# Optimization experiments

Measured on AMD Instinct MI355X. Metric: run time of the kernel, lower is better.

## Reference

```python
import jax, jax.numpy as jnp
import numpy as np

N_NODES = 100000
N_EDGES = 1600000
IN_DIM = 160
HID = 128
BN_EPS = 1e-5


def setup_inputs() -> dict:
    key = jax.random.key(0)
    ks = jax.random.split(key, 16)
    d = {}
    d['x'] = jax.random.normal(ks[0], (N_NODES, IN_DIM), dtype=jnp.float32)
    d['edge_index'] = jax.random.randint(ks[1], (2, N_EDGES), 0, N_NODES, dtype=jnp.int64)
    dims = [(IN_DIM, HID), (HID, HID), (HID, HID)]
    for i, (fi, fo) in enumerate(dims):
        s = 1.0 / np.sqrt(fi)
        d[f'wl{i}'] = jax.random.normal(ks[2 + 4 * i], (fi, fo), dtype=jnp.float32) * s
        d[f'wr{i}'] = jax.random.normal(ks[3 + 4 * i], (fi, fo), dtype=jnp.float32) * s
        d[f'bl{i}'] = jnp.zeros((fo,), dtype=jnp.float32)
        d[f'g{i}'] = jnp.ones((fo,), dtype=jnp.float32)
        d[f'be{i}'] = jnp.zeros((fo,), dtype=jnp.float32)
        d[f'rm{i}'] = jax.random.normal(ks[4 + 4 * i], (fo,), dtype=jnp.float32) * 0.1
        d[f'rv{i}'] = jnp.ones((fo,), dtype=jnp.float32)
    d['lin_w'] = jax.random.normal(ks[14], (HID, 1), dtype=jnp.float32) * (1.0 / np.sqrt(HID))
    d['lin_b'] = jnp.zeros((1,), dtype=jnp.float32)
    return d


def _sage_bn_relu(h, src, dst, wl, wr, bl, g, be, rm, rv):
    # mean neighbor aggregation: gather messages at src, scatter-mean to dst
    msg = h[src]                                            # [E, d]
    agg = jax.ops.segment_sum(msg, dst, num_segments=N_NODES)
    cnt = jax.ops.segment_sum(jnp.ones((msg.shape[0],), h.dtype), dst, num_segments=N_NODES)
    mean = agg / jnp.maximum(cnt, 1.0)[:, None]             # nodes w/o in-edges -> 0
    out = mean @ wl + bl + h @ wr                           # SAGEConv (root_weight=True)
    # BatchNorm1d (inference: running stats) + ReLU
    out = (out - rm) * (g * jax.lax.rsqrt(rv + BN_EPS)) + be
    return jax.nn.relu(out)


def reference(x, edge_index,
              wl0, wr0, bl0, g0, be0, rm0, rv0,
              wl1, wr1, bl1, g1, be1, rm1, rv1,
              wl2, wr2, bl2, g2, be2, rm2, rv2,
              lin_w, lin_b):
    src, dst = edge_index[0], edge_index[1]
    h = _sage_bn_relu(x, src, dst, wl0, wr0, bl0, g0, be0, rm0, rv0)
    h = _sage_bn_relu(h, src, dst, wl1, wr1, bl1, g1, be1, rm1, rv1)
    h = _sage_bn_relu(h, src, dst, wl2, wr2, bl2, g2, be2, rm2, rv2)
    return (h @ lin_w + lin_b)[:, 0]                        # [N]
```

## Files before the change

kernel.cpp:

```cpp
#include <hip/hip_runtime.h>

#define N_NODES 100000
#define N_EDGES 1600000
#define IN_DIM 160
#define HID 128
#define BN_EPS 1e-5f

#define M_PAD 100096
#define NBUCK 196
#define BSH 9
#define EPB 8192
#define NHB (NBUCK * NBUCK)
#define NSB 38
#define LPAD 132

typedef unsigned int uint;
typedef unsigned short ushort;
typedef __attribute__((ext_vector_type(8))) short bf16x8;
typedef __attribute__((ext_vector_type(4))) float f32x4;

__device__ __forceinline__ ushort bf16rn(float f) {
    uint u = __float_as_uint(f);
    u += 0x7fffu + ((u >> 16) & 1u);
    return (ushort)(u >> 16);
}
__device__ __forceinline__ float bflo(uint u) { return __uint_as_float(u << 16); }
__device__ __forceinline__ float bfhi(uint u) { return __uint_as_float(u & 0xffff0000u); }


__global__ __launch_bounds__(256) void hist_kernel(const int* __restrict__ dst,
                                                   int* __restrict__ ghist) {
    __shared__ int hist[NBUCK];
    int b = blockIdx.x, t = threadIdx.x;
    for (int i = t; i < NBUCK; i += 256) hist[i] = 0;
    __syncthreads();
    int e0 = b * EPB;
    for (int i = 0; i < EPB; i += 256) {
        int e = e0 + i + t;
        if (e < N_EDGES) atomicAdd(&hist[dst[e] >> BSH], 1);
    }
    __syncthreads();
    for (int i = t; i < NBUCK; i += 256) ghist[i * NBUCK + b] = hist[i];
}

__global__ __launch_bounds__(256) void scan1_kernel(const int* __restrict__ ghist,
                                                    int* __restrict__ bsum) {
    __shared__ int wsum[4];
    int b = blockIdx.x, t = threadIdx.x;
    int i4 = b * 256 + t;
    int4 v = (i4 * 4 < NHB) ? ((const int4*)ghist)[i4] : make_int4(0, 0, 0, 0);
    int s = v.x + v.y + v.z + v.w;
#pragma unroll
    for (int off = 32; off; off >>= 1) s += __shfl_down(s, off);
    if ((t & 63) == 0) wsum[t >> 6] = s;
    __syncthreads();
    if (t == 0) bsum[b] = wsum[0] + wsum[1] + wsum[2] + wsum[3];
}

__global__ void scan2_kernel(const int* __restrict__ bsum, int* __restrict__ boff,
                             int* __restrict__ gbb) {
    int lane = threadIdx.x;
    int v = (lane < NSB) ? bsum[lane] : 0;
    int s = v;
#pragma unroll
    for (int off = 1; off <= 32; off <<= 1) {
        int t2 = __shfl_up(s, off);
        if (lane >= off) s += t2;
    }
    if (lane < NSB) boff[lane] = s - v;
    if (lane == 0) gbb[NBUCK] = N_EDGES;
}

__global__ __launch_bounds__(256) void scan3_kernel(int* __restrict__ ghist,
                                                    const int* __restrict__ boff,
                                                    int* __restrict__ gbb) {
    __shared__ int ts[256];
    int b = blockIdx.x, t = threadIdx.x;
    int i4 = b * 256 + t;
    bool ok = (i4 * 4) < NHB;
    int4 v = ok ? ((const int4*)ghist)[i4] : make_int4(0, 0, 0, 0);
    int s = v.x + v.y + v.z + v.w;
    ts[t] = s;
    __syncthreads();
    for (int off = 1; off < 256; off <<= 1) {
        int a = (t >= off) ? ts[t - off] : 0;
        __syncthreads();
        ts[t] += a;
        __syncthreads();
    }
    int excl = boff[b] + ((t > 0) ? ts[t - 1] : 0);
    if (ok) {
        int idx = i4 * 4;
        int4 w;
        w.x = excl;
        w.y = excl + v.x;
        w.z = excl + v.x + v.y;
        w.w = excl + v.x + v.y + v.z;
        ((int4*)ghist)[i4] = w;
        if (idx % NBUCK == 0) gbb[idx / NBUCK] = w.x;
    }
}

__global__ __launch_bounds__(256) void scatter_kernel(const int* __restrict__ src,
                                                      const int* __restrict__ dst,
                                                      const int* __restrict__ ghist,
                                                      uint* __restrict__ scat) {
    __shared__ int base[NBUCK];
    __shared__ int fill[NBUCK];
    int b = blockIdx.x, t = threadIdx.x;
    for (int i = t; i < NBUCK; i += 256) { base[i] = ghist[i * NBUCK + b]; fill[i] = 0; }
    __syncthreads();
    int e0 = b * EPB;
    for (int i = 0; i < EPB; i += 256) {
        int e = e0 + i + t;
        if (e < N_EDGES) {
            int d = dst[e];
            int sv = src[e];
            int bk = d >> BSH;
            int lp = atomicAdd(&fill[bk], 1);
            scat[base[bk] + lp] = (uint)sv | ((uint)(d & 511) << 17);
        }
    }
}

__global__ __launch_bounds__(256) void bucket_csr_kernel(const uint* __restrict__ scat,
                                                         const int* __restrict__ gbb,
                                                         int* __restrict__ prow,
                                                         int* __restrict__ deg,
                                                         int* __restrict__ peidx) {
    __shared__ int cnt[512], fl[512], pref[512];
    __shared__ int ts[256];
    __shared__ int tot_s;
    int b = blockIdx.x, t = threadIdx.x;
    int beg = gbb[b], end = gbb[b + 1];
    int pb = beg + b * 8192;
    cnt[t] = 0; cnt[t + 256] = 0;
    __syncthreads();
    for (int i = beg + t; i < end; i += 256)
        atomicAdd(&cnt[scat[i] >> 17], 1);
    __syncthreads();
    int c0 = cnt[2 * t], c1 = cnt[2 * t + 1];
    int p0 = (c0 + 15) & ~15, p1 = (c1 + 15) & ~15;
    ts[t] = p0 + p1;
    __syncthreads();
    for (int off = 1; off < 256; off <<= 1) {
        int v = (t >= off) ? ts[t - off] : 0;
        __syncthreads();
        ts[t] += v;
        __syncthreads();
    }
    int ex = (t > 0) ? ts[t - 1] : 0;
    pref[2 * t] = ex;
    pref[2 * t + 1] = ex + p0;
    fl[t] = 0; fl[t + 256] = 0;
    if (t == 255) tot_s = ts[255];
    int g0 = b * 512 + 2 * t;
    if (g0 < N_NODES) { prow[g0] = pb + ex; deg[g0] = c0; }
    if (g0 + 1 < N_NODES) { prow[g0 + 1] = pb + ex + p0; deg[g0 + 1] = c1; }
    __syncthreads();
    int tot = tot_s;
    for (int i = t; i < tot; i += 256) peidx[pb + i] = 0;
    __syncthreads();
    for (int i = beg + t; i < end; i += 256) {
        uint w = scat[i];
        int nl = (int)(w >> 17);
        int lp = atomicAdd(&fl[nl], 1);
        peidx[pb + pref[nl] + lp] = (int)(w & 0x1FFFFu);
    }
}

__global__ void prep_weights_kernel(const float* __restrict__ wl, const float* __restrict__ wr,
                                    ushort* __restrict__ Bt, int K) {
    int n = blockIdx.y;
    int k = blockIdx.x * 64 + threadIdx.x;
    if (k < K) {
        float v = (n < HID) ? wl[k * HID + n] : wr[k * HID + (n - HID)];
        Bt[n * K + k] = bf16rn(v);
    }
}

__global__ void bn_prep_kernel(const float* __restrict__ bl0, const float* __restrict__ g0,
                               const float* __restrict__ be0, const float* __restrict__ rm0,
                               const float* __restrict__ rv0,
                               const float* __restrict__ bl1, const float* __restrict__ g1,
                               const float* __restrict__ be1, const float* __restrict__ rm1,
                               const float* __restrict__ rv1,
                               const float* __restrict__ bl2, const float* __restrict__ g2,
                               const float* __restrict__ be2, const float* __restrict__ rm2,
                               const float* __restrict__ rv2,
                               float* __restrict__ scale, float* __restrict__ shift) {
    int t = threadIdx.x;
    int L = t >> 7, j = t & 127;
    const float* bl = (L == 0) ? bl0 : (L == 1) ? bl1 : bl2;
    const float* g  = (L == 0) ? g0  : (L == 1) ? g1  : g2;
    const float* be = (L == 0) ? be0 : (L == 1) ? be1 : be2;
    const float* rm = (L == 0) ? rm0 : (L == 1) ? rm1 : rm2;
    const float* rv = (L == 0) ? rv0 : (L == 1) ? rv1 : rv2;
    float s = g[j] * rsqrtf(rv[j] + BN_EPS);
    scale[t] = s;
    shift[t] = (bl[j] - rm[j]) * s + be[j];
}

template <int K, bool AFP32>
__global__ __launch_bounds__(256) void gemm_kernel(const void* __restrict__ A_,
                                                   const ushort* __restrict__ Bt,
                                                   ushort* __restrict__ tl,
                                                   ushort* __restrict__ troot) {
    constexpr int CPR = (K * 2) / 16;
    constexpr int FULLG = CPR & ~7;
    __shared__ ushort ldsA[128 * K];
    const int t = threadIdx.x;
    const int m0b = blockIdx.x * 128;

#pragma unroll
    for (int i = 0; i < (128 * CPR) / 256; ++i) {
        int cidx = i * 256 + t;
        int row = cidx / CPR;
        int j = cidx - row * CPR;
        bf16x8 v;
        if (AFP32) {
            const float* A = (const float*)A_;
            int m = m0b + row;
            float4 f0 = make_float4(0.f, 0.f, 0.f, 0.f), f1 = f0;
            if (m < N_NODES) {
                f0 = *(const float4*)(A + (size_t)m * K + j * 8);
                f1 = *(const float4*)(A + (size_t)m * K + j * 8 + 4);
            }
            v[0] = (short)bf16rn(f0.x); v[1] = (short)bf16rn(f0.y);
            v[2] = (short)bf16rn(f0.z); v[3] = (short)bf16rn(f0.w);
            v[4] = (short)bf16rn(f1.x); v[5] = (short)bf16rn(f1.y);
            v[6] = (short)bf16rn(f1.z); v[7] = (short)bf16rn(f1.w);
        } else {
            const ushort* A = (const ushort*)A_;
            v = *(const bf16x8*)(A + (size_t)(m0b + row) * K + j * 8);
        }
        int swz = (j < FULLG) ? ((j & ~7) | ((j ^ row) & 7))
                              : ((j & ~3) | ((j ^ row) & 3));
        *(bf16x8*)&ldsA[row * K + swz * 8] = v;
    }
    __syncthreads();

    const int lane = threadIdx.x & 63;
    const int wv = threadIdx.x >> 6;
    const int col = lane & 15;
    const int q = lane >> 4;
    const int nc0 = blockIdx.y * 128;
    const int row0 = wv * 32 + col;
    f32x4 acc[2][8];
#pragma unroll
    for (int a = 0; a < 2; ++a)
#pragma unroll
        for (int tt = 0; tt < 8; ++tt) acc[a][tt] = (f32x4){0.f, 0.f, 0.f, 0.f};

#pragma unroll
    for (int k0 = 0; k0 < K; k0 += 32) {
        int jj = (k0 >> 3) + q;
        int swzj = (jj < FULLG) ? ((jj & ~7) | ((jj ^ col) & 7))
                                : ((jj & ~3) | ((jj ^ col) & 3));
        bf16x8 a0 = *(const bf16x8*)&ldsA[row0 * K + swzj * 8];
        bf16x8 a1 = *(const bf16x8*)&ldsA[(row0 + 16) * K + swzj * 8];
        int kk = k0 + q * 8;
#pragma unroll
        for (int tt = 0; tt < 8; ++tt) {
            bf16x8 bfr = *(const bf16x8*)(Bt + (size_t)(nc0 + tt * 16 + col) * K + kk);
            acc[0][tt] = __builtin_amdgcn_mfma_f32_16x16x32_bf16(a0, bfr, acc[0][tt], 0, 0, 0);
            acc[1][tt] = __builtin_amdgcn_mfma_f32_16x16x32_bf16(a1, bfr, acc[1][tt], 0, 0, 0);
        }
    }

    __syncthreads();
    ushort(*rp)[16][LPAD] = (ushort(*)[16][LPAD])ldsA;
    ushort* outp = blockIdx.y ? troot : tl;
#pragma unroll
    for (int mt = 0; mt < 2; ++mt) {
#pragma unroll
        for (int tt = 0; tt < 8; ++tt)
#pragma unroll
            for (int r = 0; r < 4; ++r)
                rp[wv][q * 4 + r][tt * 16 + col] = bf16rn(acc[mt][tt][r]);
        int mbase = blockIdx.x * 128 + wv * 32 + mt * 16;
#pragma unroll
        for (int i = 0; i < 4; ++i) {
            int lin = i * 64 + lane;
            int row = lin >> 4;
            int c16 = lin & 15;
            bf16x8 v = *(const bf16x8*)&rp[wv][row][c16 * 8];
            *(bf16x8*)(outp + (size_t)(mbase + row) * HID + c16 * 8) = v;
        }
    }
}

template <bool FINAL>
__global__ __launch_bounds__(256, 2) void agg_kernel(
    const ushort* __restrict__ tl_, const ushort* __restrict__ troot_,
    const int* __restrict__ prow, const int* __restrict__ deg_,
    const int* __restrict__ peidx,
    const float* __restrict__ bnscale, const float* __restrict__ bnshift,
    const float* __restrict__ linw, const float* __restrict__ linb,
    ushort* __restrict__ hout, float* __restrict__ out) {
    const int lane = threadIdx.x & 63;
    const int wvg = (blockIdx.x * 256 + (int)threadIdx.x) >> 6;
    const int g = lane >> 4;
    const int s = lane & 15;
    const int n = wvg * 4 + g;
    const int nn = (n < N_NODES) ? n : (N_NODES - 1);

    float4 sc0 = *(const float4*)(bnscale + s * 8);
    float4 sc1 = *(const float4*)(bnscale + s * 8 + 4);
    float4 sh0 = *(const float4*)(bnshift + s * 8);
    float4 sh1 = *(const float4*)(bnshift + s * 8 + 4);

    int pbeg = prow[nn];
    int dg = (n < N_NODES) ? deg_[nn] : 0;
    int myb = (dg + 15) >> 4;

    float acc[8];
#pragma unroll
    for (int i = 0; i < 8; ++i) acc[i] = 0.f;

    const int gsel = (lane & 48) << 2;

    for (int b = 0;; ++b) {
        bool act = b < myb;
        if (!__any(act)) break;
        int base = act ? (pbeg + b * 16) : 0;
        int idx = peidx[base + s];
        uint4 u[16];
#pragma unroll
        for (int jj = 0; jj < 16; ++jj) {
            int src = __builtin_amdgcn_ds_bpermute(gsel | (jj << 2), idx);
            src = ((b * 16 + jj) < dg) ? src : 0;
            u[jj] = *(const uint4*)(tl_ + (size_t)src * HID + s * 8);
        }
#pragma unroll
        for (int jj = 0; jj < 16; ++jj) {
            float m = ((b * 16 + jj) < dg) ? 1.f : 0.f;
            acc[0] = fmaf(m, bflo(u[jj].x), acc[0]);
            acc[1] = fmaf(m, bfhi(u[jj].x), acc[1]);
            acc[2] = fmaf(m, bflo(u[jj].y), acc[2]);
            acc[3] = fmaf(m, bfhi(u[jj].y), acc[3]);
            acc[4] = fmaf(m, bflo(u[jj].z), acc[4]);
            acc[5] = fmaf(m, bfhi(u[jj].z), acc[5]);
            acc[6] = fmaf(m, bflo(u[jj].w), acc[6]);
            acc[7] = fmaf(m, bfhi(u[jj].w), acc[7]);
        }
    }

    float inv = 1.0f / (float)((dg > 0) ? dg : 1);
    uint4 rv = *(const uint4*)(troot_ + (size_t)nn * HID + s * 8);
    float o[8];
    o[0] = fmaxf(fmaf(fmaf(acc[0], inv, bflo(rv.x)), sc0.x, sh0.x), 0.f);
    o[1] = fmaxf(fmaf(fmaf(acc[1], inv, bfhi(rv.x)), sc0.y, sh0.y), 0.f);
    o[2] = fmaxf(fmaf(fmaf(acc[2], inv, bflo(rv.y)), sc0.z, sh0.z), 0.f);
    o[3] = fmaxf(fmaf(fmaf(acc[3], inv, bfhi(rv.y)), sc0.w, sh0.w), 0.f);
    o[4] = fmaxf(fmaf(fmaf(acc[4], inv, bflo(rv.z)), sc1.x, sh1.x), 0.f);
    o[5] = fmaxf(fmaf(fmaf(acc[5], inv, bfhi(rv.z)), sc1.y, sh1.y), 0.f);
    o[6] = fmaxf(fmaf(fmaf(acc[6], inv, bflo(rv.w)), sc1.z, sh1.z), 0.f);
    o[7] = fmaxf(fmaf(fmaf(acc[7], inv, bfhi(rv.w)), sc1.w, sh1.w), 0.f);

    if (FINAL) {
        float4 w0 = *(const float4*)(linw + s * 8);
        float4 w1 = *(const float4*)(linw + s * 8 + 4);
        float p = o[0] * w0.x + o[1] * w0.y + o[2] * w0.z + o[3] * w0.w +
                  o[4] * w1.x + o[5] * w1.y + o[6] * w1.z + o[7] * w1.w;
#pragma unroll
        for (int off = 1; off < 16; off <<= 1) p += __shfl_xor(p, off);
        if (s == 0 && n < N_NODES) out[n] = p + linb[0];
    } else {
        uint4 pk;
        pk.x = (uint)bf16rn(o[0]) | ((uint)bf16rn(o[1]) << 16);
        pk.y = (uint)bf16rn(o[2]) | ((uint)bf16rn(o[3]) << 16);
        pk.z = (uint)bf16rn(o[4]) | ((uint)bf16rn(o[5]) << 16);
        pk.w = (uint)bf16rn(o[6]) | ((uint)bf16rn(o[7]) << 16);
        if (n < N_NODES) *(uint4*)(hout + (size_t)n * HID + s * 8) = pk;
    }
}


extern "C" void kernel_launch(void* const* d_in, const int* in_sizes, int n_in,
                              void* d_out, int out_size, void* d_ws, size_t ws_size,
                              hipStream_t stream) {
    const float* x    = (const float*)d_in[0];
    const int*   ei   = (const int*)d_in[1];
    const int*   esrc = ei;
    const int*   edst = ei + N_EDGES;
    const float* wl[3]; const float* wr[3]; const float* bl[3];
    const float* g[3];  const float* be[3]; const float* rm[3]; const float* rv[3];
    for (int i = 0; i < 3; ++i) {
        wl[i] = (const float*)d_in[2 + 7 * i];
        wr[i] = (const float*)d_in[3 + 7 * i];
        bl[i] = (const float*)d_in[4 + 7 * i];
        g[i]  = (const float*)d_in[5 + 7 * i];
        be[i] = (const float*)d_in[6 + 7 * i];
        rm[i] = (const float*)d_in[7 + 7 * i];
        rv[i] = (const float*)d_in[8 + 7 * i];
    }
    const float* lin_w = (const float*)d_in[23];
    const float* lin_b = (const float*)d_in[24];
    float* out = (float*)d_out;

    char* ws = (char*)d_ws;
    size_t off = 0;
    auto carve = [&](size_t bytes) -> void* {
        void* p = ws + off;
        off += (bytes + 255) & ~(size_t)255;
        return p;
    };
    int*    prow   = (int*)carve((size_t)(N_NODES + 8) * sizeof(int));
    int*    deg    = (int*)carve((size_t)(N_NODES + 8) * sizeof(int));
    int*    peidx  = (int*)carve((size_t)3210000 * sizeof(int));
    uint*   scat   = (uint*)carve((size_t)N_EDGES * sizeof(uint));
    int*    ghist  = (int*)carve((size_t)(NSB * 1024) * sizeof(int));
    int*    gbb    = (int*)carve((NBUCK + 4) * sizeof(int));
    int*    bsum   = (int*)carve((NSB + 2) * sizeof(int));
    int*    boff   = (int*)carve((NSB + 2) * sizeof(int));
    ushort* tl     = (ushort*)carve((size_t)M_PAD * HID * sizeof(ushort));
    ushort* troot  = (ushort*)carve((size_t)M_PAD * HID * sizeof(ushort));
    ushort* h      = (ushort*)carve((size_t)M_PAD * HID * sizeof(ushort));
    ushort* Bt0    = (ushort*)carve(256 * IN_DIM * sizeof(ushort));
    ushort* Bt1    = (ushort*)carve(256 * HID * sizeof(ushort));
    ushort* Bt2    = (ushort*)carve(256 * HID * sizeof(ushort));
    float*  bnsc   = (float*)carve(3 * HID * sizeof(float));
    float*  bnsh   = (float*)carve(3 * HID * sizeof(float));
    (void)ws_size; (void)n_in; (void)in_sizes; (void)out_size;

    hist_kernel<<<NBUCK, 256, 0, stream>>>(edst, ghist);
    scan1_kernel<<<NSB, 256, 0, stream>>>(ghist, bsum);
    scan2_kernel<<<1, 64, 0, stream>>>(bsum, boff, gbb);
    scan3_kernel<<<NSB, 256, 0, stream>>>(ghist, boff, gbb);
    scatter_kernel<<<NBUCK, 256, 0, stream>>>(esrc, edst, ghist, scat);
    bucket_csr_kernel<<<NBUCK, 256, 0, stream>>>(scat, gbb, prow, deg, peidx);

    prep_weights_kernel<<<dim3((IN_DIM + 63) / 64, 256), 64, 0, stream>>>(wl[0], wr[0], Bt0, IN_DIM);
    prep_weights_kernel<<<dim3((HID + 63) / 64, 256), 64, 0, stream>>>(wl[1], wr[1], Bt1, HID);
    prep_weights_kernel<<<dim3((HID + 63) / 64, 256), 64, 0, stream>>>(wl[2], wr[2], Bt2, HID);
    bn_prep_kernel<<<1, 384, 0, stream>>>(bl[0], g[0], be[0], rm[0], rv[0],
                                          bl[1], g[1], be[1], rm[1], rv[1],
                                          bl[2], g[2], be[2], rm[2], rv[2],
                                          bnsc, bnsh);

    const dim3 GEMM_GRID(M_PAD / 128, 2);
    const int AGG_GRID = (N_NODES + 15) / 16;

    gemm_kernel<IN_DIM, true><<<GEMM_GRID, 256, 0, stream>>>(x, Bt0, tl, troot);
    agg_kernel<false><<<AGG_GRID, 256, 0, stream>>>(tl, troot, prow, deg, peidx, bnsc, bnsh,
                                                    nullptr, nullptr, h, nullptr);
    gemm_kernel<HID, false><<<GEMM_GRID, 256, 0, stream>>>(h, Bt1, tl, troot);
    agg_kernel<false><<<AGG_GRID, 256, 0, stream>>>(tl, troot, prow, deg, peidx, bnsc + HID, bnsh + HID,
                                                    nullptr, nullptr, h, nullptr);
    gemm_kernel<HID, false><<<GEMM_GRID, 256, 0, stream>>>(h, Bt2, tl, troot);
    agg_kernel<true><<<AGG_GRID, 256, 0, stream>>>(tl, troot, prow, deg, peidx, bnsc + 2 * HID, bnsh + 2 * HID,
                                                   lin_w, lin_b, nullptr, out);
}
```

Measured before the change: 514.6 us.

## Compute both GEMM halves per block and drop masking in aggregation via zero sentinel row

```diff
diff --git a/kernel.cpp b/kernel.cpp
--- a/kernel.cpp
+++ b/kernel.cpp
@@ -18,6 +18,7 @@
 typedef unsigned short ushort;
 typedef __attribute__((ext_vector_type(8))) short bf16x8;
 typedef __attribute__((ext_vector_type(4))) float f32x4;
+typedef __attribute__((ext_vector_type(2))) float f32x2;
 
 __device__ __forceinline__ ushort bf16rn(float f) {
     uint u = __float_as_uint(f);
@@ -159,7 +160,7 @@
     if (g0 + 1 < N_NODES) { prow[g0 + 1] = pb + ex + p0; deg[g0 + 1] = c1; }
     __syncthreads();
     int tot = tot_s;
-    for (int i = t; i < tot; i += 256) peidx[pb + i] = 0;
+    for (int i = t; i < tot; i += 256) peidx[pb + i] = N_NODES;
     __syncthreads();
     for (int i = beg + t; i < end; i += 256) {
         uint w = scat[i];
@@ -208,12 +209,13 @@
                                                    ushort* __restrict__ troot) {
     constexpr int CPR = (K * 2) / 16;
     constexpr int FULLG = CPR & ~7;
-    __shared__ ushort ldsA[128 * K];
+    constexpr int LDSE = (64 * K > 4 * 16 * LPAD) ? 64 * K : 4 * 16 * LPAD;
+    __shared__ ushort ldsA[LDSE];
     const int t = threadIdx.x;
-    const int m0b = blockIdx.x * 128;
-
-#pragma unroll
-    for (int i = 0; i < (128 * CPR) / 256; ++i) {
+    const int m0b = blockIdx.x * 64;
+
+#pragma unroll
+    for (int i = 0; i < (64 * CPR) / 256; ++i) {
         int cidx = i * 256 + t;
         int row = cidx / CPR;
         int j = cidx - row * CPR;
@@ -244,13 +246,10 @@
     const int wv = threadIdx.x >> 6;
     const int col = lane & 15;
     const int q = lane >> 4;
-    const int nc0 = blockIdx.y * 128;
-    const int row0 = wv * 32 + col;
-    f32x4 acc[2][8];
-#pragma unroll
-    for (int a = 0; a < 2; ++a)
-#pragma unroll
-        for (int tt = 0; tt < 8; ++tt) acc[a][tt] = (f32x4){0.f, 0.f, 0.f, 0.f};
+    const int row0 = wv * 16 + col;
+    f32x4 acc[16];
+#pragma unroll
+    for (int tt = 0; tt < 16; ++tt) acc[tt] = (f32x4){0.f, 0.f, 0.f, 0.f};
 
 #pragma unroll
     for (int k0 = 0; k0 < K; k0 += 32) {
@@ -258,27 +257,25 @@
         int swzj = (jj < FULLG) ? ((jj & ~7) | ((jj ^ col) & 7))
                                 : ((jj & ~3) | ((jj ^ col) & 3));
         bf16x8 a0 = *(const bf16x8*)&ldsA[row0 * K + swzj * 8];
-        bf16x8 a1 = *(const bf16x8*)&ldsA[(row0 + 16) * K + swzj * 8];
         int kk = k0 + q * 8;
 #pragma unroll
-        for (int tt = 0; tt < 8; ++tt) {
-            bf16x8 bfr = *(const bf16x8*)(Bt + (size_t)(nc0 + tt * 16 + col) * K + kk);
-            acc[0][tt] = __builtin_amdgcn_mfma_f32_16x16x32_bf16(a0, bfr, acc[0][tt], 0, 0, 0);
-            acc[1][tt] = __builtin_amdgcn_mfma_f32_16x16x32_bf16(a1, bfr, acc[1][tt], 0, 0, 0);
+        for (int tt = 0; tt < 16; ++tt) {
+            bf16x8 bfr = *(const bf16x8*)(Bt + (size_t)(tt * 16 + col) * K + kk);
+            acc[tt] = __builtin_amdgcn_mfma_f32_16x16x32_bf16(a0, bfr, acc[tt], 0, 0, 0);
         }
     }
 
     __syncthreads();
     ushort(*rp)[16][LPAD] = (ushort(*)[16][LPAD])ldsA;
-    ushort* outp = blockIdx.y ? troot : tl;
-#pragma unroll
-    for (int mt = 0; mt < 2; ++mt) {
+#pragma unroll
+    for (int pass = 0; pass < 2; ++pass) {
+        ushort* outp = pass ? troot : tl;
 #pragma unroll
         for (int tt = 0; tt < 8; ++tt)
 #pragma unroll
             for (int r = 0; r < 4; ++r)
-                rp[wv][q * 4 + r][tt * 16 + col] = bf16rn(acc[mt][tt][r]);
-        int mbase = blockIdx.x * 128 + wv * 32 + mt * 16;
+                rp[wv][q * 4 + r][tt * 16 + col] = bf16rn(acc[pass * 8 + tt][r]);
+        int mbase = m0b + wv * 16;
 #pragma unroll
         for (int i = 0; i < 4; ++i) {
             int lin = i * 64 + lane;
@@ -291,7 +288,7 @@
 }
 
 template <bool FINAL>
-__global__ __launch_bounds__(256, 2) void agg_kernel(
+__global__ __launch_bounds__(256) void agg_kernel(
     const ushort* __restrict__ tl_, const ushort* __restrict__ troot_,
     const int* __restrict__ prow, const int* __restrict__ deg_,
     const int* __restrict__ peidx,
@@ -314,49 +311,42 @@
     int dg = (n < N_NODES) ? deg_[nn] : 0;
     int myb = (dg + 15) >> 4;
 
-    float acc[8];
-#pragma unroll
-    for (int i = 0; i < 8; ++i) acc[i] = 0.f;
+    f32x2 acc2[4];
+#pragma unroll
+    for (int i = 0; i < 4; ++i) acc2[i] = (f32x2){0.f, 0.f};
 
     const int gsel = (lane & 48) << 2;
 
     for (int b = 0;; ++b) {
         bool act = b < myb;
         if (!__any(act)) break;
-        int base = act ? (pbeg + b * 16) : 0;
-        int idx = peidx[base + s];
+        int idx = act ? peidx[pbeg + b * 16 + s] : N_NODES;
         uint4 u[16];
 #pragma unroll
         for (int jj = 0; jj < 16; ++jj) {
             int src = __builtin_amdgcn_ds_bpermute(gsel | (jj << 2), idx);
-            src = ((b * 16 + jj) < dg) ? src : 0;
             u[jj] = *(const uint4*)(tl_ + (size_t)src * HID + s * 8);
         }
 #pragma unroll
         for (int jj = 0; jj < 16; ++jj) {
-            float m = ((b * 16 + jj) < dg) ? 1.f : 0.f;
-            acc[0] = fmaf(m, bflo(u[jj].x), acc[0]);
-            acc[1] = fmaf(m, bfhi(u[jj].x), acc[1]);
-            acc[2] = fmaf(m, bflo(u[jj].y), acc[2]);
-            acc[3] = fmaf(m, bfhi(u[jj].y), acc[3]);
-            acc[4] = fmaf(m, bflo(u[jj].z), acc[4]);
-            acc[5] = fmaf(m, bfhi(u[jj].z), acc[5]);
-            acc[6] = fmaf(m, bflo(u[jj].w), acc[6]);
-            acc[7] = fmaf(m, bfhi(u[jj].w), acc[7]);
+            acc2[0] += (f32x2){bflo(u[jj].x), bfhi(u[jj].x)};
+            acc2[1] += (f32x2){bflo(u[jj].y), bfhi(u[jj].y)};
+            acc2[2] += (f32x2){bflo(u[jj].z), bfhi(u[jj].z)};
+            acc2[3] += (f32x2){bflo(u[jj].w), bfhi(u[jj].w)};
         }
     }
 
     float inv = 1.0f / (float)((dg > 0) ? dg : 1);
     uint4 rv = *(const uint4*)(troot_ + (size_t)nn * HID + s * 8);
     float o[8];
-    o[0] = fmaxf(fmaf(fmaf(acc[0], inv, bflo(rv.x)), sc0.x, sh0.x), 0.f);
-    o[1] = fmaxf(fmaf(fmaf(acc[1], inv, bfhi(rv.x)), sc0.y, sh0.y), 0.f);
-    o[2] = fmaxf(fmaf(fmaf(acc[2], inv, bflo(rv.y)), sc0.z, sh0.z), 0.f);
-    o[3] = fmaxf(fmaf(fmaf(acc[3], inv, bfhi(rv.y)), sc0.w, sh0.w), 0.f);
-    o[4] = fmaxf(fmaf(fmaf(acc[4], inv, bflo(rv.z)), sc1.x, sh1.x), 0.f);
-    o[5] = fmaxf(fmaf(fmaf(acc[5], inv, bfhi(rv.z)), sc1.y, sh1.y), 0.f);
-    o[6] = fmaxf(fmaf(fmaf(acc[6], inv, bflo(rv.w)), sc1.z, sh1.z), 0.f);
-    o[7] = fmaxf(fmaf(fmaf(acc[7], inv, bfhi(rv.w)), sc1.w, sh1.w), 0.f);
+    o[0] = fmaxf(fmaf(fmaf(acc2[0].x, inv, bflo(rv.x)), sc0.x, sh0.x), 0.f);
+    o[1] = fmaxf(fmaf(fmaf(acc2[0].y, inv, bfhi(rv.x)), sc0.y, sh0.y), 0.f);
+    o[2] = fmaxf(fmaf(fmaf(acc2[1].x, inv, bflo(rv.y)), sc0.z, sh0.z), 0.f);
+    o[3] = fmaxf(fmaf(fmaf(acc2[1].y, inv, bfhi(rv.y)), sc0.w, sh0.w), 0.f);
+    o[4] = fmaxf(fmaf(fmaf(acc2[2].x, inv, bflo(rv.z)), sc1.x, sh1.x), 0.f);
+    o[5] = fmaxf(fmaf(fmaf(acc2[2].y, inv, bfhi(rv.z)), sc1.y, sh1.y), 0.f);
+    o[6] = fmaxf(fmaf(fmaf(acc2[3].x, inv, bflo(rv.w)), sc1.z, sh1.z), 0.f);
+    o[7] = fmaxf(fmaf(fmaf(acc2[3].y, inv, bfhi(rv.w)), sc1.w, sh1.w), 0.f);
 
     if (FINAL) {
         float4 w0 = *(const float4*)(linw + s * 8);
@@ -367,12 +357,14 @@
         for (int off = 1; off < 16; off <<= 1) p += __shfl_xor(p, off);
         if (s == 0 && n < N_NODES) out[n] = p + linb[0];
     } else {
-        uint4 pk;
-        pk.x = (uint)bf16rn(o[0]) | ((uint)bf16rn(o[1]) << 16);
-        pk.y = (uint)bf16rn(o[2]) | ((uint)bf16rn(o[3]) << 16);
-        pk.z = (uint)bf16rn(o[4]) | ((uint)bf16rn(o[5]) << 16);
-        pk.w = (uint)bf16rn(o[6]) | ((uint)bf16rn(o[7]) << 16);
-        if (n < N_NODES) *(uint4*)(hout + (size_t)n * HID + s * 8) = pk;
+        uint4 pk = make_uint4(0u, 0u, 0u, 0u);
+        if (n < N_NODES) {
+            pk.x = (uint)bf16rn(o[0]) | ((uint)bf16rn(o[1]) << 16);
+            pk.y = (uint)bf16rn(o[2]) | ((uint)bf16rn(o[3]) << 16);
+            pk.z = (uint)bf16rn(o[4]) | ((uint)bf16rn(o[5]) << 16);
+            pk.w = (uint)bf16rn(o[6]) | ((uint)bf16rn(o[7]) << 16);
+        }
+        *(uint4*)(hout + (size_t)n * HID + s * 8) = pk;
     }
 }
 
@@ -414,7 +406,7 @@
     int*    gbb    = (int*)carve((NBUCK + 4) * sizeof(int));
     int*    bsum   = (int*)carve((NSB + 2) * sizeof(int));
     int*    boff   = (int*)carve((NSB + 2) * sizeof(int));
-    ushort* tl     = (ushort*)carve((size_t)M_PAD * HID * sizeof(ushort));
+    ushort* tl     = (ushort*)carve((size_t)(M_PAD + 1) * HID * sizeof(ushort));
     ushort* troot  = (ushort*)carve((size_t)M_PAD * HID * sizeof(ushort));
     ushort* h      = (ushort*)carve((size_t)M_PAD * HID * sizeof(ushort));
     ushort* Bt0    = (ushort*)carve(256 * IN_DIM * sizeof(ushort));
@@ -439,8 +431,8 @@
                                           bl[2], g[2], be[2], rm[2], rv[2],
                                           bnsc, bnsh);
 
-    const dim3 GEMM_GRID(M_PAD / 128, 2);
-    const int AGG_GRID = (N_NODES + 15) / 16;
+    const int GEMM_GRID = M_PAD / 64;
+    const int AGG_GRID = M_PAD / 16;
 
     gemm_kernel<IN_DIM, true><<<GEMM_GRID, 256, 0, stream>>>(x, Bt0, tl, troot);
     agg_kernel<false><<<AGG_GRID, 256, 0, stream>>>(tl, troot, prow, deg, peidx, bnsc, bnsh,
```

Measured after the change: 581.5 us. +13.0%, slower.
